# Optimization experiments

Measured on AMD Instinct MI355X. Metric: run time of the kernel, lower is better.

The kernel has to match this reference:

```python
import jax, jax.numpy as jnp
import numpy as np

W0, W1, W2 = 1.0, 1e-4, 1e-5  # loss_weight


def _gray_mask(imgs):
    """Emulate ToPILImage -> convert('L') -> mean-threshold point() -> ToTensor.
    imgs: [B,3,H,W] float in [0,1]. Returns binary mask in {0,1}, broadcast to [B,3,H,W].
    """
    u8 = jnp.floor(imgs * 255.0)  # ToPILImage: mul(255).byte() truncation
    # PIL L-mode: (R*299 + G*587 + B*114) / 1000, integer truncated
    gray = jnp.floor((u8[:, 0] * 299.0 + u8[:, 1] * 587.0 + u8[:, 2] * 114.0) / 1000.0)
    thres = gray.mean(axis=(1, 2), keepdims=True)  # np.array(mask).mean() per sample
    mask = jnp.where(gray > thres, 0.0, 1.0)       # point(0 if x>thres else 255) then /255
    return jnp.broadcast_to(mask[:, None], imgs.shape)


def _gradient_map(x):
    # finite-difference gradient magnitude with zero-padded shifts
    B, C, H, W = x.shape
    r = jnp.pad(x, ((0, 0), (0, 0), (0, 0), (0, 1)))[..., 1:]       # x[j+1], 0 at right edge
    l = jnp.pad(x, ((0, 0), (0, 0), (0, 0), (1, 0)))[..., :W]       # x[j-1], 0 at left edge
    t = jnp.pad(x, ((0, 0), (0, 0), (1, 0), (0, 0)))[..., :H, :]    # x[i-1], 0 at top edge
    b = jnp.pad(x, ((0, 0), (0, 0), (0, 1), (0, 0)))[..., 1:, :]    # x[i+1], 0 at bottom edge
    return jnp.sqrt(((r - l) * 0.5) ** 2 + ((t - b) * 0.5) ** 2 + 1e-6)


def setup_inputs() -> dict:
    key = jax.random.key(0)
    k1, k2, k3, k4 = jax.random.split(key, 4)
    return {
        "out_images": jax.random.uniform(k1, (128, 3, 128, 512), dtype=jnp.float32),
        "target_images": jax.random.uniform(k2, (128, 3, 128, 512), dtype=jnp.float32),
        "text_pred": jax.random.normal(k3, (4096, 10000), dtype=jnp.float32),
        "text_gt": jax.random.randint(k4, (4096,), 0, 10000, dtype=jnp.int64),
    }


def reference(out_images, target_images, text_pred, text_gt):
    # l2: MSE over images
    l2 = jnp.mean((out_images - target_images) ** 2)
    # lg: L1 between gradient maps of binarized masks (masks are detached: built via PIL)
    mo = jax.lax.stop_gradient(_gray_mask(out_images))
    mt = jax.lax.stop_gradient(_gray_mask(target_images))
    lg = jnp.mean(jnp.abs(_gradient_map(mo) - _gradient_map(mt)))
    # lce: mean cross-entropy
    logp = jax.nn.log_softmax(text_pred, axis=-1)
    ce = -jnp.mean(jnp.take_along_axis(logp, text_gt[:, None], axis=-1))
    return W0 * l2 + W1 * lg + W2 * ce
```

## Files before the change

### kernel.cpp

```cpp
#include <hip/hip_runtime.h>
#include <hip/hip_bf16.h>
#include <math.h>

#define BB 128
#define HH 128
#define WW 512
#define HW (HH*WW)
#define NPIX ((size_t)BB*HW)
#define ROWS 4096
#define COLS 10000
#define P1_BLOCKS (BB*16)
#define LCE_BLOCKS (ROWS/4)


__device__ __forceinline__ int gray_of(float r, float g, float b) {
    int ri = (int)floorf(r * 255.0f);
    int gi = (int)floorf(g * 255.0f);
    int bi = (int)floorf(b * 255.0f);
    return (299 * ri + 587 * gi + 114 * bi) / 1000;
}

template <bool STORE_GRAY>
__global__ __launch_bounds__(256) void fused1_kernel(
    const float* __restrict__ outI, const float* __restrict__ tgtI,
    const float* __restrict__ X, const int* __restrict__ gt,
    float* __restrict__ l2p, int* __restrict__ gso, int* __restrict__ gst,
    float* __restrict__ cep,
    unsigned char* __restrict__ gout, unsigned char* __restrict__ gtgt) {
    const int tid = threadIdx.x;
    const int bid = blockIdx.x;

    if (bid < P1_BLOCKS) {
        const int b     = bid >> 4;
        const int chunk = bid & 15;
        const float4* o4 = (const float4*)(outI + (size_t)b * 3 * HW) + chunk * 1024;
        const float4* t4 = (const float4*)(tgtI + (size_t)b * 3 * HW) + chunk * 1024;
        uchar4* go4 = (uchar4*)(gout + (size_t)b * HW) + chunk * 1024;
        uchar4* gt4 = (uchar4*)(gtgt + (size_t)b * HW) + chunk * 1024;

        float l2 = 0.0f;
        int so = 0, st = 0;
#pragma unroll
        for (int k = 0; k < 4; ++k) {
            int v = tid + k * 256;
            float4 oR = o4[v], oG = o4[v + HW/4], oB = o4[v + 2*(HW/4)];
            float4 tR = t4[v], tG = t4[v + HW/4], tB = t4[v + 2*(HW/4)];
            float d;
            d = oR.x-tR.x; l2 += d*d;  d = oR.y-tR.y; l2 += d*d;
            d = oR.z-tR.z; l2 += d*d;  d = oR.w-tR.w; l2 += d*d;
            d = oG.x-tG.x; l2 += d*d;  d = oG.y-tG.y; l2 += d*d;
            d = oG.z-tG.z; l2 += d*d;  d = oG.w-tG.w; l2 += d*d;
            d = oB.x-tB.x; l2 += d*d;  d = oB.y-tB.y; l2 += d*d;
            d = oB.z-tB.z; l2 += d*d;  d = oB.w-tB.w; l2 += d*d;

            int g0 = gray_of(oR.x, oG.x, oB.x);
            int g1 = gray_of(oR.y, oG.y, oB.y);
            int g2 = gray_of(oR.z, oG.z, oB.z);
            int g3 = gray_of(oR.w, oG.w, oB.w);
            so += g0 + g1 + g2 + g3;
            if (STORE_GRAY) go4[v] = make_uchar4((unsigned char)g0,(unsigned char)g1,(unsigned char)g2,(unsigned char)g3);
            g0 = gray_of(tR.x, tG.x, tB.x);
            g1 = gray_of(tR.y, tG.y, tB.y);
            g2 = gray_of(tR.z, tG.z, tB.z);
            g3 = gray_of(tR.w, tG.w, tB.w);
            st += g0 + g1 + g2 + g3;
            if (STORE_GRAY) gt4[v] = make_uchar4((unsigned char)g0,(unsigned char)g1,(unsigned char)g2,(unsigned char)g3);
        }

        __shared__ float sl2[256];
        __shared__ int s1[256], s2[256];
        sl2[tid] = l2; s1[tid] = so; s2[tid] = st;
        __syncthreads();
        for (int off = 128; off > 0; off >>= 1) {
            if (tid < off) { sl2[tid] += sl2[tid+off]; s1[tid] += s1[tid+off]; s2[tid] += s2[tid+off]; }
            __syncthreads();
        }
        if (tid == 0) { l2p[bid] = sl2[0]; gso[bid] = s1[0]; gst[bid] = s2[0]; }
    } else {
        const int wid = tid >> 6, lane = tid & 63;
        const int row = (bid - P1_BLOCKS) * 4 + wid;
        const float4* xr = (const float4*)(X + (size_t)row * COLS);

        float s0 = 0.0f, s1 = 0.0f;
        const int NV = COLS / 4;
        for (int v = lane; v < NV; v += 64) {
            float4 x = xr[v];
            s0 += __expf(x.x) + __expf(x.y);
            s1 += __expf(x.z) + __expf(x.w);
        }
        float s = s0 + s1;
        for (int off = 32; off > 0; off >>= 1) s += __shfl_down(s, off);
        if (lane == 0) {
            float xg = X[(size_t)row * COLS + gt[row]];
            cep[row] = __logf(s) - xg;
        }
    }
}

__device__ __forceinline__ int mask8(uint2 v, int ti) {
    int m = 0;
#pragma unroll
    for (int k = 0; k < 4; ++k) m |= (((int)((v.x >> (8*k)) & 255) <= ti) ? 1 : 0) << k;
#pragma unroll
    for (int k = 0; k < 4; ++k) m |= (((int)((v.y >> (8*k)) & 255) <= ti) ? 1 : 0) << (k+4);
    return m;
}

__device__ __forceinline__ void grad_bits(const unsigned char* __restrict__ G,
                                          int r, int roff, int ti, int lane,
                                          int& ax, int& vy) {
    uint2 cc = *(const uint2*)(G + roff);
    uint2 aa = *(const uint2*)(G + (r > 0   ? roff - 512 : roff));
    uint2 bb = *(const uint2*)(G + (r < 127 ? roff + 512 : roff));
    int mc = mask8(cc, ti);
    int ma = (r > 0)   ? mask8(aa, ti) : 0;
    int mb = (r < 127) ? mask8(bb, ti) : 0;
    int prev = __shfl_up(mc, 1);
    int next = __shfl_down(mc, 1);
    int lb = ((mc << 1) & 0xFF) | ((lane > 0)  ? ((prev >> 7) & 1) : 0);
    int rb = (mc >> 1)          | ((lane < 63) ? ((next & 1) << 7) : 0);
    ax = lb ^ rb;
    vy = ma ^ mb;
}

__global__ __launch_bounds__(256) void pass2_kernel(
    const unsigned char* __restrict__ gout, const unsigned char* __restrict__ gtgt,
    const int* __restrict__ gso, const int* __restrict__ gst,
    float* __restrict__ lgp) {
    const int tid  = threadIdx.x;
    const int wave = tid >> 6, lane = tid & 63;
    const int b  = blockIdx.x >> 4;
    const int rg = blockIdx.x & 15;

    int s_o = 0, s_t = 0;
#pragma unroll
    for (int k = 0; k < 16; ++k) { s_o += gso[b*16 + k]; s_t += gst[b*16 + k]; }
    const int ti_o = s_o >> 16;
    const int ti_t = s_t >> 16;
    const unsigned char* Go = gout + (size_t)b * HW;
    const unsigned char* Gt = gtgt + (size_t)b * HW;

    const float v0 = sqrtf(1e-6f);
    const float v1 = sqrtf(0.25f + 1e-6f);
    const float v2 = sqrtf(0.5f + 1e-6f);

    float sum = 0.0f;
#pragma unroll
    for (int rr = 0; rr < 2; ++rr) {
        const int r = rg * 8 + wave * 2 + rr;
        const int roff = r * 512 + lane * 8;
        int ax_o, vy_o, ax_t, vy_t;
        grad_bits(Go, r, roff, ti_o, lane, ax_o, vy_o);
        grad_bits(Gt, r, roff, ti_t, lane, ax_t, vy_t);
#pragma unroll
        for (int k = 0; k < 8; ++k) {
            int so = ((ax_o >> k) & 1) + ((vy_o >> k) & 1);
            int st = ((ax_t >> k) & 1) + ((vy_t >> k) & 1);
            float g_o = (so == 0) ? v0 : ((so == 1) ? v1 : v2);
            float g_t = (st == 0) ? v0 : ((st == 1) ? v1 : v2);
            sum += fabsf(g_o - g_t);
        }
    }

    for (int off = 32; off > 0; off >>= 1) sum += __shfl_down(sum, off);
    __shared__ float ws4[4];
    if (lane == 0) ws4[wave] = sum;
    __syncthreads();
    if (tid == 0) lgp[blockIdx.x] = ws4[0] + ws4[1] + ws4[2] + ws4[3];
}

__device__ __forceinline__ float mask_at(const float* __restrict__ img, size_t base, int p, float thres) {
    float r = img[base + p], g = img[base + p + HW], b = img[base + p + 2*HW];
    return ((float)gray_of(r, g, b) > thres) ? 0.0f : 1.0f;
}

__global__ __launch_bounds__(256) void pass2_recompute_kernel(
    const float* __restrict__ outI, const float* __restrict__ tgtI,
    const int* __restrict__ gso, const int* __restrict__ gst,
    float* __restrict__ lgp) {
    const int tid   = threadIdx.x;
    const int b     = blockIdx.x >> 4;
    const int chunk = blockIdx.x & 15;
    int s_o = 0, s_t = 0;
    for (int k = 0; k < 16; ++k) { s_o += gso[b*16 + k]; s_t += gst[b*16 + k]; }
    const float to = (float)s_o * (1.0f/65536.0f);
    const float tt = (float)s_t * (1.0f/65536.0f);
    const size_t baseO = (size_t)b * 3 * HW;

    float sum = 0.0f;
    for (int u = 0; u < 16; ++u) {
        int p = chunk * 4096 + u * 256 + tid;
        int i = p >> 9, j = p & 511;
        float mr = (j+1 < WW) ? mask_at(outI, baseO, p+1,  to) : 0.0f;
        float ml = (j-1 >= 0) ? mask_at(outI, baseO, p-1,  to) : 0.0f;
        float mt = (i-1 >= 0) ? mask_at(outI, baseO, p-WW, to) : 0.0f;
        float mb = (i+1 < HH) ? mask_at(outI, baseO, p+WW, to) : 0.0f;
        float dx = (mr - ml) * 0.5f, dy = (mt - mb) * 0.5f;
        float gmo = sqrtf(dx*dx + dy*dy + 1e-6f);
        mr = (j+1 < WW) ? mask_at(tgtI, baseO, p+1,  tt) : 0.0f;
        ml = (j-1 >= 0) ? mask_at(tgtI, baseO, p-1,  tt) : 0.0f;
        mt = (i-1 >= 0) ? mask_at(tgtI, baseO, p-WW, tt) : 0.0f;
        mb = (i+1 < HH) ? mask_at(tgtI, baseO, p+WW, tt) : 0.0f;
        dx = (mr - ml) * 0.5f; dy = (mt - mb) * 0.5f;
        float gmt = sqrtf(dx*dx + dy*dy + 1e-6f);
        sum += fabsf(gmo - gmt);
    }

    __shared__ float sred[256];
    sred[tid] = sum;
    __syncthreads();
    for (int off = 128; off > 0; off >>= 1) {
        if (tid < off) sred[tid] += sred[tid+off];
        __syncthreads();
    }
    if (tid == 0) lgp[blockIdx.x] = sred[0];
}

__global__ __launch_bounds__(256) void combine_kernel(
    const float* __restrict__ l2p, const float* __restrict__ lgp,
    const float* __restrict__ cep, float* __restrict__ out) {
    __shared__ double s0[256], s1[256], s2[256];
    const int t = threadIdx.x;
    double a = 0.0, bsum = 0.0, c = 0.0;
    for (int i = t; i < 2048; i += 256) { a += (double)l2p[i]; bsum += (double)lgp[i]; }
    for (int i = t; i < 4096; i += 256) c += (double)cep[i];
    s0[t] = a; s1[t] = bsum; s2[t] = c;
    __syncthreads();
    for (int off = 128; off > 0; off >>= 1) {
        if (t < off) { s0[t] += s0[t+off]; s1[t] += s1[t+off]; s2[t] += s2[t+off]; }
        __syncthreads();
    }
    if (t == 0) {
        double l2 = s0[0] / (double)(3.0 * (double)NPIX);
        double lg = s1[0] / (double)NPIX;
        double ce = s2[0] / (double)ROWS;
        out[0] = (float)(l2 + 1e-4 * lg + 1e-5 * ce);
    }
}

extern "C" void kernel_launch(void* const* d_in, const int* in_sizes, int n_in,
                              void* d_out, int out_size, void* d_ws, size_t ws_size,
                              hipStream_t stream) {
    const float* outI = (const float*)d_in[0];
    const float* tgtI = (const float*)d_in[1];
    const float* X    = (const float*)d_in[2];
    const int*   gt   = (const int*)d_in[3];

    float* l2p = (float*)d_ws;
    int*   gso = (int*)((char*)d_ws + 8192);
    int*   gst = (int*)((char*)d_ws + 16384);
    float* lgp = (float*)((char*)d_ws + 24576);
    float* cep = (float*)((char*)d_ws + 32768);
    unsigned char* gray = (unsigned char*)d_ws + 65536;
    const size_t need = 65536 + 2 * NPIX;
    const bool useCache = ws_size >= need;

    if (useCache) {
        fused1_kernel<true><<<P1_BLOCKS + LCE_BLOCKS, 256, 0, stream>>>(
            outI, tgtI, X, gt, l2p, gso, gst, cep, gray, gray + NPIX);
        pass2_kernel<<<BB * 16, 256, 0, stream>>>(gray, gray + NPIX, gso, gst, lgp);
    } else {
        fused1_kernel<false><<<P1_BLOCKS + LCE_BLOCKS, 256, 0, stream>>>(
            outI, tgtI, X, gt, l2p, gso, gst, cep, gray, gray);
        pass2_recompute_kernel<<<BB * 16, 256, 0, stream>>>(outI, tgtI, gso, gst, lgp);
    }
    combine_kernel<<<1, 256, 0, stream>>>(l2p, lgp, cep, (float*)d_out);
}
```

Before: 97.59 us.

## Interleave image and cross-entropy blocks, batch loads, use shuffle reductions

Reorders the fused grid so every third block handles cross-entropy rows while the rest process image chunks, mixing the two workloads across the GPU. Image blocks now issue all twelve float4 loads per tensor before computing, for more memory-level parallelism. The shared-memory tree reduction becomes wave shuffles plus a four-entry combine. The logsumexp loop is manually unrolled with four independent loads per iteration. Register pressure rises from holding 24 float4 values per thread.

```diff
diff --git a/kernel.cpp b/kernel.cpp
--- a/kernel.cpp
+++ b/kernel.cpp
@@ -11,6 +11,7 @@
 #define COLS 10000
 #define P1_BLOCKS (BB*16)
 #define LCE_BLOCKS (ROWS/4)
+#define GRID (P1_BLOCKS + LCE_BLOCKS)
 
 
 __device__ __forceinline__ int gray_of(float r, float g, float b) {
@@ -18,6 +19,10 @@
     int gi = (int)floorf(g * 255.0f);
     int bi = (int)floorf(b * 255.0f);
     return (299 * ri + 587 * gi + 114 * bi) / 1000;
+}
+
+__device__ __forceinline__ float e4(float4 x) {
+    return (__expf(x.x) + __expf(x.y)) + (__expf(x.z) + __expf(x.w));
 }
 
 template <bool STORE_GRAY>
@@ -29,22 +34,35 @@
     unsigned char* __restrict__ gout, unsigned char* __restrict__ gtgt) {
     const int tid = threadIdx.x;
     const int bid = blockIdx.x;
-
-    if (bid < P1_BLOCKS) {
-        const int b     = bid >> 4;
-        const int chunk = bid & 15;
+    const int wid = tid >> 6, lane = tid & 63;
+
+    if ((bid % 3) != 2) {
+        const int p1    = 2 * (bid / 3) + (bid % 3);
+        const int b     = p1 >> 4;
+        const int chunk = p1 & 15;
         const float4* o4 = (const float4*)(outI + (size_t)b * 3 * HW) + chunk * 1024;
         const float4* t4 = (const float4*)(tgtI + (size_t)b * 3 * HW) + chunk * 1024;
         uchar4* go4 = (uchar4*)(gout + (size_t)b * HW) + chunk * 1024;
         uchar4* gt4 = (uchar4*)(gtgt + (size_t)b * HW) + chunk * 1024;
 
+        float4 o[12], t[12];
+#pragma unroll
+        for (int k = 0; k < 4; ++k) {
+            int v = tid + k * 256;
+            o[3*k+0] = o4[v]; o[3*k+1] = o4[v + HW/4]; o[3*k+2] = o4[v + 2*(HW/4)];
+        }
+#pragma unroll
+        for (int k = 0; k < 4; ++k) {
+            int v = tid + k * 256;
+            t[3*k+0] = t4[v]; t[3*k+1] = t4[v + HW/4]; t[3*k+2] = t4[v + 2*(HW/4)];
+        }
+
         float l2 = 0.0f;
         int so = 0, st = 0;
 #pragma unroll
         for (int k = 0; k < 4; ++k) {
-            int v = tid + k * 256;
-            float4 oR = o4[v], oG = o4[v + HW/4], oB = o4[v + 2*(HW/4)];
-            float4 tR = t4[v], tG = t4[v + HW/4], tB = t4[v + 2*(HW/4)];
+            float4 oR = o[3*k], oG = o[3*k+1], oB = o[3*k+2];
+            float4 tR = t[3*k], tG = t[3*k+1], tB = t[3*k+2];
             float d;
             d = oR.x-tR.x; l2 += d*d;  d = oR.y-tR.y; l2 += d*d;
             d = oR.z-tR.z; l2 += d*d;  d = oR.w-tR.w; l2 += d*d;
@@ -58,37 +76,45 @@
             int g2 = gray_of(oR.z, oG.z, oB.z);
             int g3 = gray_of(oR.w, oG.w, oB.w);
             so += g0 + g1 + g2 + g3;
-            if (STORE_GRAY) go4[v] = make_uchar4((unsigned char)g0,(unsigned char)g1,(unsigned char)g2,(unsigned char)g3);
+            if (STORE_GRAY) go4[tid + k*256] = make_uchar4((unsigned char)g0,(unsigned char)g1,(unsigned char)g2,(unsigned char)g3);
             g0 = gray_of(tR.x, tG.x, tB.x);
             g1 = gray_of(tR.y, tG.y, tB.y);
             g2 = gray_of(tR.z, tG.z, tB.z);
             g3 = gray_of(tR.w, tG.w, tB.w);
             st += g0 + g1 + g2 + g3;
-            if (STORE_GRAY) gt4[v] = make_uchar4((unsigned char)g0,(unsigned char)g1,(unsigned char)g2,(unsigned char)g3);
-        }
-
-        __shared__ float sl2[256];
-        __shared__ int s1[256], s2[256];
-        sl2[tid] = l2; s1[tid] = so; s2[tid] = st;
+            if (STORE_GRAY) gt4[tid + k*256] = make_uchar4((unsigned char)g0,(unsigned char)g1,(unsigned char)g2,(unsigned char)g3);
+        }
+
+        for (int off = 32; off > 0; off >>= 1) {
+            l2 += __shfl_down(l2, off);
+            so += __shfl_down(so, off);
+            st += __shfl_down(st, off);
+        }
+        __shared__ float wl2[4];
+        __shared__ int w1[4], w2[4];
+        if (lane == 0) { wl2[wid] = l2; w1[wid] = so; w2[wid] = st; }
         __syncthreads();
-        for (int off = 128; off > 0; off >>= 1) {
-            if (tid < off) { sl2[tid] += sl2[tid+off]; s1[tid] += s1[tid+off]; s2[tid] += s2[tid+off]; }
-            __syncthreads();
-        }
-        if (tid == 0) { l2p[bid] = sl2[0]; gso[bid] = s1[0]; gst[bid] = s2[0]; }
+        if (tid == 0) {
+            l2p[p1] = wl2[0] + wl2[1] + wl2[2] + wl2[3];
+            gso[p1] = w1[0] + w1[1] + w1[2] + w1[3];
+            gst[p1] = w2[0] + w2[1] + w2[2] + w2[3];
+        }
     } else {
-        const int wid = tid >> 6, lane = tid & 63;
-        const int row = (bid - P1_BLOCKS) * 4 + wid;
+        const int row = (bid / 3) * 4 + wid;
         const float4* xr = (const float4*)(X + (size_t)row * COLS);
 
-        float s0 = 0.0f, s1 = 0.0f;
-        const int NV = COLS / 4;
-        for (int v = lane; v < NV; v += 64) {
-            float4 x = xr[v];
-            s0 += __expf(x.x) + __expf(x.y);
-            s1 += __expf(x.z) + __expf(x.w);
-        }
-        float s = s0 + s1;
+        float s = 0.0f;
+        int v = lane;
+#pragma unroll
+        for (int k = 0; k < 9; ++k, v += 256) {
+            float4 a = xr[v], b2 = xr[v+64], c = xr[v+128], d = xr[v+192];
+            s += e4(a) + e4(b2) + e4(c) + e4(d);
+        }
+        {
+            float4 a = xr[v], b2 = xr[v+64], c = xr[v+128];
+            s += e4(a) + e4(b2) + e4(c);
+            if (v + 192 < COLS/4) s += e4(xr[v+192]);
+        }
         for (int off = 32; off > 0; off >>= 1) s += __shfl_down(s, off);
         if (lane == 0) {
             float xg = X[(size_t)row * COLS + gt[row]];
@@ -256,11 +282,11 @@
     const bool useCache = ws_size >= need;
 
     if (useCache) {
-        fused1_kernel<true><<<P1_BLOCKS + LCE_BLOCKS, 256, 0, stream>>>(
+        fused1_kernel<true><<<GRID, 256, 0, stream>>>(
             outI, tgtI, X, gt, l2p, gso, gst, cep, gray, gray + NPIX);
         pass2_kernel<<<BB * 16, 256, 0, stream>>>(gray, gray + NPIX, gso, gst, lgp);
     } else {
-        fused1_kernel<false><<<P1_BLOCKS + LCE_BLOCKS, 256, 0, stream>>>(
+        fused1_kernel<false><<<GRID, 256, 0, stream>>>(
             outI, tgtI, X, gt, l2p, gso, gst, cep, gray, gray);
         pass2_recompute_kernel<<<BB * 16, 256, 0, stream>>>(outI, tgtI, gso, gst, lgp);
     }
```

Result: no change. 98.18 us (+0.6%).
